# Optimization experiments

Measured on AMD Instinct MI355X. Metric: run time of the kernel, lower is better.

The kernel has to match this reference:

```python
import jax, jax.numpy as jnp
import numpy as np

EPS = 1e-5  # BatchNorm2d default eps

def setup_inputs() -> dict:
    key = jax.random.key(0)
    k1, k2, k3, k4 = jax.random.split(key, 4)
    B, Cin, Cout, T, V = 64, 64, 128, 300, 25
    x = jax.random.normal(k1, (B, Cin, T, V), dtype=jnp.float32)
    adj = jax.random.uniform(k2, (V, V), dtype=jnp.float32)
    # Conv2d(kernel_size=1) weight (Cout, Cin), kaiming-ish scale
    W = jax.random.normal(k3, (Cout, Cin), dtype=jnp.float32) * (1.0 / np.sqrt(Cin))
    b = jnp.zeros((Cout,), dtype=jnp.float32)
    gamma = jnp.ones((Cout,), dtype=jnp.float32)
    beta = jnp.zeros((Cout,), dtype=jnp.float32)
    return {"x": x, "adj": adj, "W": W, "b": b, "gamma": gamma, "beta": beta}

def reference(x, adj, W, b, gamma, beta):
    # x: (B, C, T, V); graph aggregation over joints: matmul with adj on last dim
    xg = jnp.einsum('bctv,vw->bctw', x, adj)
    # 1x1 conv == per-(t,v) channel projection
    y = jnp.einsum('bctv,oc->botv', xg, W) + b[None, :, None, None]
    # BatchNorm2d (training mode): per-channel stats over (B, T, V), biased var
    mean = jnp.mean(y, axis=(0, 2, 3), keepdims=True)
    var = jnp.mean((y - mean) ** 2, axis=(0, 2, 3), keepdims=True)
    yn = (y - mean) * jax.lax.rsqrt(var + EPS)
    out = jax.nn.relu(gamma[None, :, None, None] * yn + beta[None, :, None, None])
    return out
```

## Files before the change

### kernel.cpp

```cpp
#include <hip/hip_runtime.h>
#include <hip/hip_bf16.h>
#include <stdint.h>

typedef __attribute__((ext_vector_type(8)))  short    short8;
typedef __attribute__((ext_vector_type(16))) float    floatx16;
typedef __attribute__((ext_vector_type(4)))  float    floatx4;
typedef __attribute__((ext_vector_type(4)))  uint32_t uint4v;

#define B_    64
#define CIN   64
#define COUT  128
#define T_    300
#define V_    25
#define NRED  (B_ * T_ * V_)
#define NSLOTS 32
#define NT    12
#define EPS   1e-5f

__device__ __forceinline__ uint32_t pk2(float a, float b) {
    union { __hip_bfloat162 h; uint32_t u; } c;
    c.h = __float22bfloat162_rn(make_float2(a, b));
    return c.u;
}

__device__ __forceinline__ floatx16 fzero16() {
    floatx16 z;
#pragma unroll
    for (int i = 0; i < 16; ++i) z[i] = 0.f;
    return z;
}

__device__ __forceinline__ int div25(int n) { return (n * 5243) >> 17; }

__device__ __forceinline__ void cvt_hb(const floatx16 h, int q, short8 hb[2]) {
    uint32_t pk[8], pp[8];
#pragma unroll
    for (int i = 0; i < 8; ++i) pk[i] = pk2(h[2 * i], h[2 * i + 1]);
#pragma unroll
    for (int i = 0; i < 8; ++i) pp[i] = (uint32_t)__shfl_xor((int)pk[i], 32, 64);
#pragma unroll
    for (int s = 0; s < 2; ++s) {
        union { short8 sv; uint32_t u[4]; } F;
        F.u[0] = q ? pp[4 * s + 2] : pk[4 * s];
        F.u[1] = q ? pp[4 * s + 3] : pk[4 * s + 1];
        F.u[2] = q ? pk[4 * s + 2] : pp[4 * s];
        F.u[3] = q ? pk[4 * s + 3] : pp[4 * s + 1];
        hb[s] = F.sv;
    }
}

__device__ __forceinline__ void build_const_frags(const float* __restrict__ W,
                                                  const float* __restrict__ adj,
                                                  int wave, int ln, int q,
                                                  short8 wf[4], short8 af[2]) {
    const float* wr = W + (32 * wave + ln) * CIN;
#pragma unroll
    for (int kk = 0; kk < 4; ++kk) {
        int c0 = 16 * kk + 8 * q;
        floatx4 a = *(const floatx4*)(wr + c0);
        floatx4 b = *(const floatx4*)(wr + c0 + 4);
        union { short8 sv; uint32_t u[4]; } F;
        F.u[0] = pk2(a[0], a[1]); F.u[1] = pk2(a[2], a[3]);
        F.u[2] = pk2(b[0], b[1]); F.u[3] = pk2(b[2], b[3]);
        wf[kk] = F.sv;
    }
#pragma unroll
    for (int s = 0; s < 2; ++s) {
        union { short8 sv; uint32_t u[4]; } F;
#pragma unroll
        for (int p = 0; p < 4; ++p) {
            int v0 = 16 * s + 8 * q + 2 * p;
            float e0 = (v0     < V_ && ln < V_) ? adj[v0 * V_ + ln]       : 0.f;
            float e1 = (v0 + 1 < V_ && ln < V_) ? adj[(v0 + 1) * V_ + ln] : 0.f;
            F.u[p] = pk2(e0, e1);
        }
        af[s] = F.sv;
    }
}

__device__ __forceinline__ void stage_issue(const float* __restrict__ xb, int t4,
                                            int tid, floatx4 a[4], floatx4 b[4]) {
#pragma unroll
    for (int i = 0; i < 4; ++i) {
        int cid = i * 256 + tid;
        if (i < 3 || tid < 32) {
            int ch = cid >> 5;
            int cp = cid & 31;
            const float* p0 = xb + (2 * cp) * 7500 + t4 * 25 + 4 * ch;
            a[i] = *(const floatx4*)p0;
            b[i] = *(const floatx4*)(p0 + 7500);
        }
    }
}

__device__ __forceinline__ void stage_commit(uint32_t* __restrict__ lds, int tid,
                                             const floatx4 a[4], const floatx4 b[4]) {
#pragma unroll
    for (int i = 0; i < 4; ++i) {
        int cid = i * 256 + tid;
        if (i < 3 || tid < 32) {
            int ch = cid >> 5;
            int cp = cid & 31;
            const int g  = cp >> 2;
            const int c2 = cp & 3;
#pragma unroll
            for (int k = 0; k < 4; ++k) {
                int tv = 4 * ch + k;
                lds[tv * 32 + (((g ^ (tv & 7)) << 2) | c2)] = pk2(a[i][k], b[i][k]);
            }
        }
    }
}

__device__ __forceinline__ void build_xa_ldsT(const uint32_t* __restrict__ lds,
                                              int tloc, int vcl, int q, short8 xa[4]) {
    const int tv = tloc * 25 + vcl;
    const uint32_t* row = lds + tv * 32;
    const int x7 = tv & 7;
#pragma unroll
    for (int kk = 0; kk < 4; ++kk) {
        union { short8 sv; uint4v u4; } F;
        F.u4 = *(const uint4v*)(row + (((q + 2 * kk) ^ x7) << 2));
        xa[kk] = F.sv;
    }
}

__device__ __forceinline__ floatx16 compute_yt(const short8 xa[4], const short8 wf[4],
                                               const short8 af[2], int q) {
    floatx16 h = fzero16();
#pragma unroll
    for (int kk = 0; kk < 4; ++kk)
        h = __builtin_amdgcn_mfma_f32_32x32x16_bf16(xa[kk], wf[kk], h, 0, 0, 0);
    short8 hb[2];
    cvt_hb(h, q, hb);
    floatx16 y = fzero16();
#pragma unroll
    for (int s = 0; s < 2; ++s)
        y = __builtin_amdgcn_mfma_f32_32x32x16_bf16(af[s], hb[s], y, 0, 0, 0);
    return y;
}

__global__ __launch_bounds__(256, 3) void pass1_kernel(
    const float* __restrict__ x, const float* __restrict__ adj,
    const float* __restrict__ W,
    float* __restrict__ psum, float* __restrict__ psq)
{
    __shared__ __attribute__((aligned(16))) uint32_t bufA[3200];
    __shared__ __attribute__((aligned(16))) uint32_t bufB[3200];

    const int tid  = threadIdx.x;
    const int wave = tid >> 6;
    const int lane = tid & 63;
    const int q    = lane >> 5;
    const int ln   = lane & 31;
    const int b    = blockIdx.y;
    const int tbase = blockIdx.x * NT;

    short8 wf[4], af[2];
    build_const_frags(W, adj, wave, ln, q, wf, af);
    const int vcl = ln < V_ ? ln : V_ - 1;
    const float* xb = x + (size_t)b * (CIN * T_ * V_);

    floatx4 sa[4], sb[4];
    stage_issue(xb, tbase, tid, sa, sb);
    stage_commit(bufA, tid, sa, sb);
    __syncthreads();
    uint32_t* cur = bufA;
    uint32_t* nxt = bufB;

    float sum = 0.f, sq = 0.f;
    for (int g = 0; g < NT / 4; ++g) {
        if (g < NT / 4 - 1) stage_issue(xb, tbase + 4 * (g + 1), tid, sa, sb);
        __builtin_amdgcn_sched_barrier(0);
#pragma unroll
        for (int tloc = 0; tloc < 4; ++tloc) {
            short8 xa[4];
            build_xa_ldsT(cur, tloc, vcl, q, xa);
            floatx16 y = compute_yt(xa, wf, af, q);
#pragma unroll
            for (int r = 0; r < 16; ++r) { sum += y[r]; sq += y[r] * y[r]; }
        }
        if (g < NT / 4 - 1) {
            stage_commit(nxt, tid, sa, sb);
            __syncthreads();
            uint32_t* t = cur; cur = nxt; nxt = t;
        }
    }

    sum += __shfl_xor(sum, 32, 64);
    sq  += __shfl_xor(sq,  32, 64);
    if (q == 0) {
        int slot = (blockIdx.y * 25 + blockIdx.x) & (NSLOTS - 1);
        atomicAdd(&psum[slot * COUT + 32 * wave + ln], sum);
        atomicAdd(&psq [slot * COUT + 32 * wave + ln], sq);
    }
}

__global__ __launch_bounds__(256, 2) void pass2_kernel(
    const float* __restrict__ x, const float* __restrict__ adj,
    const float* __restrict__ W,
    const float* __restrict__ gamma, const float* __restrict__ beta,
    const float* __restrict__ psum, const float* __restrict__ psq,
    float* __restrict__ out)
{
    __shared__ __attribute__((aligned(16))) uint32_t bufA[3200];
    __shared__ __attribute__((aligned(16))) uint32_t bufB[3200];
    __shared__ __attribute__((aligned(16))) float ldso[4][3200];

    const int tid  = threadIdx.x;
    const int wave = tid >> 6;
    const int lane = tid & 63;
    const int q    = lane >> 5;
    const int ln   = lane & 31;
    const int b    = blockIdx.y;
    const int tbase = blockIdx.x * NT;
    const int o_l  = 32 * wave + ln;

    short8 wf[4], af[2];
    build_const_frags(W, adj, wave, ln, q, wf, af);

    float s = 0.f, ss = 0.f;
#pragma unroll 4
    for (int k = 0; k < NSLOTS; ++k) {
        s  += psum[k * COUT + o_l];
        ss += psq [k * COUT + o_l];
    }
    const float mean = s / (float)NRED;
    const float var  = ss / (float)NRED - mean * mean;
    const float inv  = rsqrtf(var + EPS);
    const float sc   = gamma[o_l] * inv;
    const float sh   = beta[o_l] - mean * sc;

    const int vcl = ln < V_ ? ln : V_ - 1;
    const float* xb = x + (size_t)b * (CIN * T_ * V_);
    float* const ob = out + (size_t)(b * COUT + 32 * wave) * (T_ * V_);

    floatx4 sa[4], sb[4];
    stage_issue(xb, tbase, tid, sa, sb);
    stage_commit(bufA, tid, sa, sb);
    __syncthreads();
    uint32_t* cur = bufA;
    uint32_t* nxt = bufB;

    for (int g = 0; g < NT / 4; ++g) {
        const int t4 = tbase + 4 * g;
        if (g < NT / 4 - 1) stage_issue(xb, tbase + 4 * (g + 1), tid, sa, sb);
        __builtin_amdgcn_sched_barrier(0);

        float* const ow0 = &ldso[wave][ln * 100];
#pragma unroll
        for (int tloc = 0; tloc < 4; ++tloc) {
            short8 xa[4];
            build_xa_ldsT(cur, tloc, vcl, q, xa);
            floatx16 y = compute_yt(xa, wf, af, q);
            float* ow = ow0 + tloc * 25 + 4 * q;
#pragma unroll
            for (int g2 = 0; g2 < 3; ++g2) {
#pragma unroll
                for (int j = 0; j < 4; ++j) {
                    float v = sc * y[4 * g2 + j] + sh;
                    ow[8 * g2 + j] = v > 0.f ? v : 0.f;
                }
            }
            if (q == 0) {
                float v = sc * y[12] + sh;
                ow0[tloc * 25 + 24] = v > 0.f ? v : 0.f;
            }
        }

        if (g < NT / 4 - 1) {
            stage_commit(nxt, tid, sa, sb);
            __syncthreads();
        }

#pragma unroll
        for (int f = 0; f < 13; ++f) {
            int cid = f * 64 + lane;
            if (f < 12 || lane < 32) {
                int o = div25(cid);
                int c = cid - 25 * o;
                floatx4 v = *(const floatx4*)&ldso[wave][o * 100 + 4 * c];
                *(floatx4*)(ob + (size_t)o * (T_ * V_) + t4 * 25 + 4 * c) = v;
            }
        }

        uint32_t* t = cur; cur = nxt; nxt = t;
    }
}


extern "C" void kernel_launch(void* const* d_in, const int* in_sizes, int n_in,
                              void* d_out, int out_size, void* d_ws, size_t ws_size,
                              hipStream_t stream) {
    const float* x     = (const float*)d_in[0];
    const float* adj   = (const float*)d_in[1];
    const float* W     = (const float*)d_in[2];
    const float* gamma = (const float*)d_in[4];
    const float* beta  = (const float*)d_in[5];
    float* out = (float*)d_out;

    float* psum = (float*)d_ws;
    float* psq  = (float*)((char*)d_ws + NSLOTS * COUT * sizeof(float));

    hipMemsetAsync(psum, 0, 2 * NSLOTS * COUT * sizeof(float), stream);

    dim3 grid(T_ / NT, B_);
    pass1_kernel<<<grid, 256, 0, stream>>>(x, adj, W, psum, psq);
    pass2_kernel<<<grid, 256, 0, stream>>>(x, adj, W, gamma, beta, psum, psq, out);
}
```

Measured before the change: 446.4 us.

## Compute BN stats via Gram matrix of graph-aggregated input instead of full projection

The stats pass no longer computes the full 128-channel projection. It forms the aggregated input Q = x·adj, accumulates the 64x64 Gram matrix QᵀQ and the channel sums of Q with MFMA, and atomically reduces them into slots. A new single-block stats kernel then derives each output channel's mean and variance as W·sum and wᵀMw, and writes scale and shift for pass2. This removes most of pass1's MFMA work, at the cost of an extra launch, a serial single-block reduction, and bf16 rounding inside the Gram products, which affects variance precision.

```diff
diff --git a/kernel.cpp b/kernel.cpp
--- a/kernel.cpp
+++ b/kernel.cpp
@@ -13,8 +13,11 @@
 #define T_    300
 #define V_    25
 #define NRED  (B_ * T_ * V_)
-#define NSLOTS 32
 #define NT    12
+#define NTC1  5
+#define NT1   (T_ / NTC1)
+#define MSLOTS 16
+#define MSTRIDE 3200
 #define EPS   1e-5f
 
 __device__ __forceinline__ uint32_t pk2(float a, float b) {
@@ -49,10 +52,24 @@
     }
 }
 
-__device__ __forceinline__ void build_const_frags(const float* __restrict__ W,
-                                                  const float* __restrict__ adj,
-                                                  int wave, int ln, int q,
-                                                  short8 wf[4], short8 af[2]) {
+__device__ __forceinline__ void build_af(const float* __restrict__ adj,
+                                         int ln, int q, short8 af[2]) {
+#pragma unroll
+    for (int s = 0; s < 2; ++s) {
+        union { short8 sv; uint32_t u[4]; } F;
+#pragma unroll
+        for (int p = 0; p < 4; ++p) {
+            int v0 = 16 * s + 8 * q + 2 * p;
+            float e0 = (v0     < V_ && ln < V_) ? adj[v0 * V_ + ln]       : 0.f;
+            float e1 = (v0 + 1 < V_ && ln < V_) ? adj[(v0 + 1) * V_ + ln] : 0.f;
+            F.u[p] = pk2(e0, e1);
+        }
+        af[s] = F.sv;
+    }
+}
+
+__device__ __forceinline__ void build_wf(const float* __restrict__ W,
+                                         int wave, int ln, int q, short8 wf[4]) {
     const float* wr = W + (32 * wave + ln) * CIN;
 #pragma unroll
     for (int kk = 0; kk < 4; ++kk) {
@@ -64,17 +81,193 @@
         F.u[2] = pk2(b[0], b[1]); F.u[3] = pk2(b[2], b[3]);
         wf[kk] = F.sv;
     }
-#pragma unroll
-    for (int s = 0; s < 2; ++s) {
-        union { short8 sv; uint32_t u[4]; } F;
-#pragma unroll
-        for (int p = 0; p < 4; ++p) {
-            int v0 = 16 * s + 8 * q + 2 * p;
-            float e0 = (v0     < V_ && ln < V_) ? adj[v0 * V_ + ln]       : 0.f;
-            float e1 = (v0 + 1 < V_ && ln < V_) ? adj[(v0 + 1) * V_ + ln] : 0.f;
-            F.u[p] = pk2(e0, e1);
-        }
-        af[s] = F.sv;
+}
+
+__device__ __forceinline__ void stage1_issue(const float* __restrict__ xb, int t4,
+                                             int tid, floatx4 st[7]) {
+#pragma unroll
+    for (int i = 0; i < 7; ++i) {
+        int cid = i * 256 + tid;
+        if (i < 6 || tid < 64) {
+            int c = div25(cid), ch = cid - 25 * c;
+            st[i] = *(const floatx4*)(xb + c * 7500 + t4 * 25 + 4 * ch);
+        }
+    }
+}
+
+__device__ __forceinline__ void stage1_commit(float* __restrict__ buf, int tid,
+                                              const floatx4 st[7]) {
+#pragma unroll
+    for (int i = 0; i < 7; ++i) {
+        int cid = i * 256 + tid;
+        if (i < 6 || tid < 64) {
+            int c = div25(cid), ch = cid - 25 * c;
+#pragma unroll
+            for (int k = 0; k < 4; ++k) {
+                int tv = 4 * ch + k;
+                int tl = div25(tv);
+                int v  = tv - 25 * tl;
+                buf[(c * 4 + tl) * 32 + (((v >> 2) ^ (c & 7)) << 2) + (v & 3)] =
+                    st[i][k];
+            }
+        }
+    }
+}
+
+__global__ __launch_bounds__(256, 2) void pass1_kernel(
+    const float* __restrict__ x, const float* __restrict__ adj,
+    float* __restrict__ wsM)
+{
+    __shared__ __attribute__((aligned(16))) float ldsx[2][8192];
+
+    const int tid  = threadIdx.x;
+    const int wave = tid >> 6;
+    const int lane = tid & 63;
+    const int q    = lane >> 5;
+    const int ln   = lane & 31;
+    const int b    = blockIdx.y;
+    const int tbase = blockIdx.x * NT1;
+
+    short8 af[2];
+    build_af(adj, ln, q, af);
+    const float* xb = x + (size_t)b * (CIN * T_ * V_);
+
+    for (int k = tid; k < 2 * 256 * 7; k += 256) {
+        int v   = 25 + (k % 7);
+        int row = (k / 7) & 255;
+        int bf  = k / (7 * 256);
+        int c   = row >> 2;
+        ldsx[bf][row * 32 + (((v >> 2) ^ (c & 7)) << 2) + (v & 3)] = 0.f;
+    }
+
+    floatx4 st[7];
+    stage1_issue(xb, tbase, tid, st);
+    stage1_commit(&ldsx[0][0], tid, st);
+    __syncthreads();
+    int cur = 0;
+
+    floatx16 M00 = fzero16(), M01 = fzero16(), M11 = fzero16();
+    float qs0 = 0.f, qs1 = 0.f;
+    const int x7 = ln & 7;
+
+    for (int g = 0; g < NT1 / 4; ++g) {
+        if (g < NT1 / 4 - 1) stage1_issue(xb, tbase + 4 * (g + 1), tid, st);
+        __builtin_amdgcn_sched_barrier(0);
+
+        const float* bufp = &ldsx[cur][0];
+        short8 xf0[2], xf1[2];
+#pragma unroll
+        for (int s = 0; s < 2; ++s) {
+            const int gb = 4 * s + 2 * q;
+#pragma unroll
+            for (int cT = 0; cT < 2; ++cT) {
+                const float* row = bufp + ((32 * cT + ln) * 4 + wave) * 32;
+                floatx4 u  = *(const floatx4*)(row + ((gb ^ x7) << 2));
+                floatx4 v4 = *(const floatx4*)(row + (((gb + 1) ^ x7) << 2));
+                union { short8 sv; uint32_t uu[4]; } F;
+                F.uu[0] = pk2(u[0], u[1]);  F.uu[1] = pk2(u[2], u[3]);
+                F.uu[2] = pk2(v4[0], v4[1]); F.uu[3] = pk2(v4[2], v4[3]);
+                if (cT == 0) xf0[s] = F.sv; else xf1[s] = F.sv;
+            }
+        }
+        floatx16 qt0 = fzero16(), qt1 = fzero16();
+        qt0 = __builtin_amdgcn_mfma_f32_32x32x16_bf16(af[0], xf0[0], qt0, 0, 0, 0);
+        qt0 = __builtin_amdgcn_mfma_f32_32x32x16_bf16(af[1], xf0[1], qt0, 0, 0, 0);
+        qt1 = __builtin_amdgcn_mfma_f32_32x32x16_bf16(af[0], xf1[0], qt1, 0, 0, 0);
+        qt1 = __builtin_amdgcn_mfma_f32_32x32x16_bf16(af[1], xf1[1], qt1, 0, 0, 0);
+#pragma unroll
+        for (int r = 0; r < 16; ++r) { qs0 += qt0[r]; qs1 += qt1[r]; }
+        short8 qb0[2], qb1[2];
+        cvt_hb(qt0, q, qb0);
+        cvt_hb(qt1, q, qb1);
+#pragma unroll
+        for (int s = 0; s < 2; ++s) {
+            M00 = __builtin_amdgcn_mfma_f32_32x32x16_bf16(qb0[s], qb0[s], M00, 0, 0, 0);
+            M01 = __builtin_amdgcn_mfma_f32_32x32x16_bf16(qb0[s], qb1[s], M01, 0, 0, 0);
+            M11 = __builtin_amdgcn_mfma_f32_32x32x16_bf16(qb1[s], qb1[s], M11, 0, 0, 0);
+        }
+
+        if (g < NT1 / 4 - 1) {
+            stage1_commit(&ldsx[cur ^ 1][0], tid, st);
+            __syncthreads();
+            cur ^= 1;
+        }
+    }
+
+    qs0 += __shfl_xor(qs0, 32, 64);
+    qs1 += __shfl_xor(qs1, 32, 64);
+    const int slot = (blockIdx.y * NTC1 + blockIdx.x) & (MSLOTS - 1);
+    float* mb = wsM + slot * MSTRIDE;
+#pragma unroll
+    for (int r = 0; r < 16; ++r) {
+        const int crow = (r & 3) + 8 * (r >> 2) + 4 * q;
+        atomicAdd(&mb[       crow * 32 + ln], M00[r]);
+        atomicAdd(&mb[1024 + crow * 32 + ln], M01[r]);
+        atomicAdd(&mb[2048 + crow * 32 + ln], M11[r]);
+    }
+    if (q == 0) {
+        atomicAdd(&mb[3072 + ln],      qs0);
+        atomicAdd(&mb[3072 + 32 + ln], qs1);
+    }
+}
+
+__global__ __launch_bounds__(256) void stats_kernel(
+    const float* __restrict__ W, const float* __restrict__ gamma,
+    const float* __restrict__ beta, const float* __restrict__ wsM,
+    float* __restrict__ wsStats)
+{
+    __shared__ float Ms[3136];
+    __shared__ float red[256];
+    const int tid = threadIdx.x;
+    for (int e = tid; e < 3136; e += 256) {
+        float a = 0.f;
+#pragma unroll
+        for (int s = 0; s < MSLOTS; ++s) a += wsM[s * MSTRIDE + e];
+        Ms[e] = a;
+    }
+    __syncthreads();
+
+    const int o = tid & 127;
+    const int h = tid >> 7;
+    float wrow[64];
+#pragma unroll
+    for (int c = 0; c < 64; ++c) wrow[c] = W[o * 64 + c];
+
+    float ss = 0.f;
+    if (h == 0) {
+#pragma unroll
+        for (int ci = 0; ci < 32; ++ci) {
+            float inner = 0.f;
+#pragma unroll
+            for (int cp = 0; cp < 32; ++cp)
+                inner += Ms[ci * 32 + cp] * wrow[cp]
+                       + Ms[1024 + ci * 32 + cp] * wrow[32 + cp];
+            ss += wrow[ci] * inner;
+        }
+    } else {
+#pragma unroll
+        for (int ci = 0; ci < 32; ++ci) {
+            float inner = 0.f;
+#pragma unroll
+            for (int cp = 0; cp < 32; ++cp)
+                inner += Ms[1024 + cp * 32 + ci] * wrow[cp]
+                       + Ms[2048 + ci * 32 + cp] * wrow[32 + cp];
+            ss += wrow[32 + ci] * inner;
+        }
+    }
+    red[tid] = ss;
+    __syncthreads();
+    if (tid < 128) {
+        const float sst = red[tid] + red[tid + 128];
+        float S = 0.f;
+#pragma unroll
+        for (int c = 0; c < 64; ++c) S += wrow[c] * Ms[3072 + c];
+        const float mean = S / (float)NRED;
+        const float var  = sst / (float)NRED - mean * mean;
+        const float inv  = rsqrtf(var + EPS);
+        const float sc   = gamma[o] * inv;
+        wsStats[o]       = sc;
+        wsStats[128 + o] = beta[o] - mean * sc;
     }
 }
 
@@ -140,67 +333,10 @@
     return y;
 }
 
-__global__ __launch_bounds__(256, 3) void pass1_kernel(
-    const float* __restrict__ x, const float* __restrict__ adj,
-    const float* __restrict__ W,
-    float* __restrict__ psum, float* __restrict__ psq)
-{
-    __shared__ __attribute__((aligned(16))) uint32_t bufA[3200];
-    __shared__ __attribute__((aligned(16))) uint32_t bufB[3200];
-
-    const int tid  = threadIdx.x;
-    const int wave = tid >> 6;
-    const int lane = tid & 63;
-    const int q    = lane >> 5;
-    const int ln   = lane & 31;
-    const int b    = blockIdx.y;
-    const int tbase = blockIdx.x * NT;
-
-    short8 wf[4], af[2];
-    build_const_frags(W, adj, wave, ln, q, wf, af);
-    const int vcl = ln < V_ ? ln : V_ - 1;
-    const float* xb = x + (size_t)b * (CIN * T_ * V_);
-
-    floatx4 sa[4], sb[4];
-    stage_issue(xb, tbase, tid, sa, sb);
-    stage_commit(bufA, tid, sa, sb);
-    __syncthreads();
-    uint32_t* cur = bufA;
-    uint32_t* nxt = bufB;
-
-    float sum = 0.f, sq = 0.f;
-    for (int g = 0; g < NT / 4; ++g) {
-        if (g < NT / 4 - 1) stage_issue(xb, tbase + 4 * (g + 1), tid, sa, sb);
-        __builtin_amdgcn_sched_barrier(0);
-#pragma unroll
-        for (int tloc = 0; tloc < 4; ++tloc) {
-            short8 xa[4];
-            build_xa_ldsT(cur, tloc, vcl, q, xa);
-            floatx16 y = compute_yt(xa, wf, af, q);
-#pragma unroll
-            for (int r = 0; r < 16; ++r) { sum += y[r]; sq += y[r] * y[r]; }
-        }
-        if (g < NT / 4 - 1) {
-            stage_commit(nxt, tid, sa, sb);
-            __syncthreads();
-            uint32_t* t = cur; cur = nxt; nxt = t;
-        }
-    }
-
-    sum += __shfl_xor(sum, 32, 64);
-    sq  += __shfl_xor(sq,  32, 64);
-    if (q == 0) {
-        int slot = (blockIdx.y * 25 + blockIdx.x) & (NSLOTS - 1);
-        atomicAdd(&psum[slot * COUT + 32 * wave + ln], sum);
-        atomicAdd(&psq [slot * COUT + 32 * wave + ln], sq);
-    }
-}
-
 __global__ __launch_bounds__(256, 2) void pass2_kernel(
     const float* __restrict__ x, const float* __restrict__ adj,
     const float* __restrict__ W,
-    const float* __restrict__ gamma, const float* __restrict__ beta,
-    const float* __restrict__ psum, const float* __restrict__ psq,
+    const float* __restrict__ wsStats,
     float* __restrict__ out)
 {
     __shared__ __attribute__((aligned(16))) uint32_t bufA[3200];
@@ -217,19 +353,11 @@
     const int o_l  = 32 * wave + ln;
 
     short8 wf[4], af[2];
-    build_const_frags(W, adj, wave, ln, q, wf, af);
-
-    float s = 0.f, ss = 0.f;
-#pragma unroll 4
-    for (int k = 0; k < NSLOTS; ++k) {
-        s  += psum[k * COUT + o_l];
-        ss += psq [k * COUT + o_l];
-    }
-    const float mean = s / (float)NRED;
-    const float var  = ss / (float)NRED - mean * mean;
-    const float inv  = rsqrtf(var + EPS);
-    const float sc   = gamma[o_l] * inv;
-    const float sh   = beta[o_l] - mean * sc;
+    build_wf(W, wave, ln, q, wf);
+    build_af(adj, ln, q, af);
+
+    const float sc = wsStats[o_l];
+    const float sh = wsStats[128 + o_l];
 
     const int vcl = ln < V_ ? ln : V_ - 1;
     const float* xb = x + (size_t)b * (CIN * T_ * V_);
@@ -287,7 +415,6 @@
         uint32_t* t = cur; cur = nxt; nxt = t;
     }
 }
-
 
 extern "C" void kernel_launch(void* const* d_in, const int* in_sizes, int n_in,
                               void* d_out, int out_size, void* d_ws, size_t ws_size,
@@ -299,12 +426,12 @@
     const float* beta  = (const float*)d_in[5];
     float* out = (float*)d_out;
 
-    float* psum = (float*)d_ws;
-    float* psq  = (float*)((char*)d_ws + NSLOTS * COUT * sizeof(float));
-
-    hipMemsetAsync(psum, 0, 2 * NSLOTS * COUT * sizeof(float), stream);
-
-    dim3 grid(T_ / NT, B_);
-    pass1_kernel<<<grid, 256, 0, stream>>>(x, adj, W, psum, psq);
-    pass2_kernel<<<grid, 256, 0, stream>>>(x, adj, W, gamma, beta, psum, psq, out);
-}
+    float* wsM     = (float*)d_ws;
+    float* wsStats = wsM + MSLOTS * MSTRIDE;
+
+    hipMemsetAsync(wsM, 0, MSLOTS * MSTRIDE * sizeof(float), stream);
+
+    pass1_kernel<<<dim3(NTC1, B_), 256, 0, stream>>>(x, adj, wsM);
+    stats_kernel<<<dim3(1), 256, 0, stream>>>(W, gamma, beta, wsM, wsStats);
+    pass2_kernel<<<dim3(T_ / NT, B_), 256, 0, stream>>>(x, adj, W, wsStats, out);
+}
```

Measured after the change: 462.6 us. 3.6% more time.
